# Optimization experiments

Hardware: AMD Instinct MI355X
Metric: run time of the kernel (lower is better)

The kernel has to match this reference:

```python
import jax, jax.numpy as jnp
import numpy as np
from jax import lax

THETA = 1.0      # neuron['theta']
TAU_SR = 10.0    # neuron['tauSr'] (SRM synaptic time constant)
TAU_RHO = 1.0    # surrogate-gradient width
SCALE_RHO = 1.0  # surrogate-gradient scale
T_SIM = 100      # simulation['tSample']


def srm_kernel(T, dtype=jnp.float32):
    t = jnp.arange(T, dtype=dtype)
    return (t / TAU_SR) * jnp.exp(1.0 - t / TAU_SR)  # eps(0)=0, peak 1 at t=tau


def psp(x, eps):
    """Causal temporal filter along last axis: y[t] = sum_k eps[k] * x[t-k]."""
    shape = x.shape
    T = shape[-1]
    xf = x.reshape(-1, 1, T)
    k = eps[::-1].reshape(1, 1, T)
    y = lax.conv_general_dilated(xf, k, (1,), [(T - 1, 0)],
                                 dimension_numbers=('NCH', 'OIH', 'NCH'))
    return y.reshape(shape)


def spike(u):
    return (u >= THETA).astype(u.dtype)


def conv_t(x, w, pad):
    """Per-timestep 2D conv. x:[B,C,H,W,T], w:[O,I,kh,kw] -> [B,O,H',W',T]."""
    B, C, H, W, T = x.shape
    xt = jnp.moveaxis(x, -1, 1).reshape(B * T, C, H, W)
    y = lax.conv_general_dilated(xt, w, (1, 1), [(pad, pad), (pad, pad)],
                                 dimension_numbers=('NCHW', 'OIHW', 'NCHW'))
    O, Ho, Wo = y.shape[1], y.shape[2], y.shape[3]
    return jnp.moveaxis(y.reshape(B, T, O, Ho, Wo), 1, -1)


def pool2(x):
    """SLAYER pool: 2x2 sum with fixed weight 1.1. x:[B,C,H,W,T]."""
    B, C, H, W, T = x.shape
    xr = x.reshape(B, C, H // 2, 2, W // 2, 2, T)
    return 1.1 * xr.sum(axis=(3, 5))


def dense_t(x, w):
    """x:[B,C,H,W,T] flattened over CHW; w:[O, C*H*W] -> [B,O,T]."""
    B = x.shape[0]
    T = x.shape[-1]
    xf = x.reshape(B, -1, T)
    return jnp.einsum('bit,oi->bot', xf, w)


def setup_inputs() -> dict:
    key = jax.random.key(0)
    k = jax.random.split(key, 6)
    img = jax.random.uniform(k[0], (32, 1, 28, 28), dtype=jnp.float32)
    rand_u = jax.random.uniform(k[1], (32, 1, 28, 28, T_SIM), dtype=jnp.float32)
    w1 = jax.random.normal(k[2], (16, 1, 5, 5), dtype=jnp.float32) * 0.2
    w2 = jax.random.normal(k[3], (32, 16, 5, 5), dtype=jnp.float32) * 0.05
    wf1 = jax.random.normal(k[4], (410, 1568), dtype=jnp.float32) * 0.05
    wf2 = jax.random.normal(k[5], (10, 410), dtype=jnp.float32) * 0.05
    return {"img": img, "rand_u": rand_u, "w1": w1, "w2": w2, "wf1": wf1, "wf2": wf2}


def reference(img, rand_u, w1, w2, wf1, wf2):
    eps = srm_kernel(T_SIM, img.dtype)
    # rate encoding: Bernoulli spikes with p = pixel intensity
    x = (rand_u < img[..., None]).astype(img.dtype)          # [B,1,28,28,T]
    x = spike(psp(conv_t(x, w1, 2), eps))                    # [B,16,28,28,T]
    x = spike(psp(pool2(x), eps))                            # [B,16,14,14,T]
    x = spike(psp(conv_t(x, w2, 2), eps))                    # [B,32,14,14,T]
    x = spike(psp(pool2(x), eps))                            # [B,32,7,7,T]
    x = spike(psp(dense_t(x, wf1), eps))                     # [B,410,T]
    x = spike(psp(jnp.einsum('bit,oi->bot', x, wf2), eps))   # [B,10,T]
    return x
```

## Files before the change

kernel.cpp:

```cpp
#include <hip/hip_runtime.h>


namespace {
constexpr int B = 32, T = 100;
constexpr double A1 = 0.90483741803595957;
constexpr double CE = 0.27182818284590452;
constexpr double SC39 = 549755813888.0;
constexpr double INV39 = 1.0 / 549755813888.0;

constexpr size_t OFF_M1 = 0;
constexpr size_t OFF_M2 = OFF_M1 + (size_t)B * T * 28 * 4;
constexpr size_t OFF_S4 = OFF_M2 + (size_t)B * T * 224 * 4;
constexpr size_t OFF_D5 = OFF_S4 + (size_t)B * T * 1568;
constexpr size_t OFF_S5 = OFF_D5 + (size_t)B * T * 410 * 8;
constexpr size_t OFF_D6 = OFF_S5 + (size_t)B * T * 410;
constexpr size_t OFF_BP = OFF_D6 + (size_t)B * T * 10 * 8;
constexpr size_t OFF_AP = OFF_D5;
}

using i32x4 = __attribute__((ext_vector_type(4))) int;
using i32x16 = __attribute__((ext_vector_type(16))) int;

__global__ void k_encode_pack(const float* __restrict__ img, const float* __restrict__ ru,
                              unsigned int* __restrict__ m1) {
  int i = blockIdx.x * 256 + threadIdx.x;
  if (i >= B * 28 * T) return;
  int t = i % T;
  int y = (i / T) % 28;
  int b = i / (T * 28);
  unsigned int m = 0;
  const float* rb = ru + ((size_t)b * 784 + y * 28) * T + t;
  const float* ib = img + b * 784 + y * 28;
  for (int x = 0; x < 28; x++) {
    m |= (rb[(size_t)x * T] < ib[x]) ? (1u << x) : 0u;
  }
  m1[((size_t)b * T + t) * 28 + y] = m;
}

__global__ __launch_bounds__(256) void k_conv1w(const unsigned int* __restrict__ m1,
                                                const float* __restrict__ w1,
                                                unsigned int* __restrict__ m2) {
  __shared__ double lut2[320 * 2];
  __shared__ unsigned int mrow[2][32];
  int o = blockIdx.x % 16, b = blockIdx.x / 16;
  int tid = threadIdx.x;
  for (int e = tid; e < 320; e += 256) {
    int dy = e / 64, f = e % 64;
    const float* wb = w1 + o * 25 + dy * 5;
    double v0 = 0.0, v1 = 0.0;
#pragma unroll
    for (int dx = 0; dx < 5; dx++) {
      double wv = (double)wb[dx];
      if ((f >> dx) & 1) v0 += wv;
      if ((f >> (dx + 1)) & 1) v1 += wv;
    }
    lut2[e * 2 + 0] = v0;
    lut2[e * 2 + 1] = v1;
  }
  if (tid < 32) {
    mrow[0][tid] = 0;
    mrow[1][tid] = 0;
  }
  int py = tid >> 4, px = tid & 15;
  bool act = (px < 14) && (py < 14);
  int yA = 2 * py, xA = 2 * px;
  double g1[4] = {0, 0, 0, 0}, g2[4] = {0, 0, 0, 0};
  double q1 = 0.0, q2 = 0.0;
  const unsigned int* m1b = m1 + (size_t)b * T * 28;
  if (tid < 28) mrow[0][tid + 2] = m1b[tid] << 2;
  __syncthreads();
  for (int t = 0; t < T; t++) {
    int p = t & 1, np = p ^ 1;
    bool dold = (tid < 28) && (t + 1 < T);
    unsigned int ldv = 0;
    if (dold) ldv = m1b[(t + 1) * 28 + tid] << 2;
    unsigned int poolBit = 0;
    if (act) {
      double sAa = 0, sAb = 0, sBa = 0, sBb = 0;
      const unsigned int* mc = mrow[p];
#pragma unroll
      for (int dy = 0; dy < 5; dy++) {
        unsigned int mA = mc[yA + dy];
        unsigned int mB = mc[yA + 1 + dy];
        const double* eA = lut2 + (dy * 64 + (int)((mA >> xA) & 63u)) * 2;
        const double* eB = lut2 + (dy * 64 + (int)((mB >> xA) & 63u)) * 2;
        sAa += eA[0];
        sAb += eA[1];
        sBa += eB[0];
        sBb += eB[1];
      }
      g1[0] = sAa + A1 * g1[0]; g2[0] = g1[0] + A1 * g2[0];
      g1[1] = sAb + A1 * g1[1]; g2[1] = g1[1] + A1 * g2[1];
      g1[2] = sBa + A1 * g1[2]; g2[2] = g1[2] + A1 * g2[2];
      g1[3] = sBb + A1 * g1[3]; g2[3] = g1[3] + A1 * g2[3];
      int s0 = (CE * (g2[0] - g1[0]) >= 1.0) ? 1 : 0;
      int s1 = (CE * (g2[1] - g1[1]) >= 1.0) ? 1 : 0;
      int s2 = (CE * (g2[2] - g1[2]) >= 1.0) ? 1 : 0;
      int s3 = (CE * (g2[3] - g1[3]) >= 1.0) ? 1 : 0;
      double s = 1.1 * (double)(s0 + s1 + s2 + s3);
      q1 = s + A1 * q1;
      q2 = q1 + A1 * q2;
      poolBit = (CE * (q2 - q1) >= 1.0) ? 1u : 0u;
    }
    unsigned long long bal = __ballot((int)poolBit);
    if (act && px == 0) {
      int lane = tid & 63;
      unsigned int rm = (unsigned int)((bal >> (lane & 48)) & 0x3FFFull);
      m2[((size_t)(b * T + t) * 16 + o) * 14 + py] = rm;
    }
    if (dold) mrow[np][tid + 2] = ldv;
    __syncthreads();
  }
}

__global__ void k_limbs(const float* __restrict__ w2, signed char* __restrict__ AP) {
  int i = blockIdx.x * 256 + threadIdx.x;
  if (i >= 32 * 80 * 8) return;
  int dx = i & 7;
  int g = (i >> 3) % 80;
  int o = i / 640;
  int c = g >> 2, r = g & 3, eh = r >> 1, kh = r & 1;
  int lane = kh * 32 + o, e = eh * 8 + dx;
  int ci = g / 5, dy = g % 5;
  float wv = (dx < 5) ? w2[((o * 16 + ci) * 5 + dy) * 5 + dx] : 0.0f;
  long long m = llrint((double)wv * SC39);
#pragma unroll
  for (int j = 0; j < 5; j++) {
    int d = (int)((m + 128) & 255) - 128;
    AP[(size_t)((j * 20 + c) * 64 + lane) * 16 + e] = (signed char)d;
    m = (m - d) >> 8;
  }
}

__global__ __launch_bounds__(512, 2) void k_conv2w(const unsigned int* __restrict__ m2,
                                                   const signed char* __restrict__ AP,
                                                   unsigned char* __restrict__ s4) {
  __shared__ unsigned int maskW[2][2][192];
  __shared__ double part[2][4][32][30];
  int yp = blockIdx.x % 7, b = blockIdx.x / 7;
  int y0 = yp * 2;
  int tid = threadIdx.x;
  int w = tid >> 6, l = tid & 63;
  int tp = w & 1, kq = w >> 1;
  int col = l & 31, kh = l >> 5;
  int x = col % 14;
  unsigned int wmask = (col < 28) ? 31u : 0u;
  int half = (col >= 14) ? 1 : 0;
  const unsigned int* m2b = m2 + (size_t)b * T * 224;

  const i32x4* APv = (const i32x4*)AP;
  i32x4 Af[5][5];
#pragma unroll
  for (int j = 0; j < 5; j++)
#pragma unroll
    for (int q = 0; q < 5; q++)
      Af[j][q] = APv[(size_t)(j * 20 + 5 * kq + q) * 64 + l];

  int stPos[3] = {-1, -1, -1}, stIdx[3] = {-1, -1, -1};
  if (w < 2) {
#pragma unroll
    for (int pass = 0; pass < 3; pass++) {
      if (pass == 2 && l >= 32) continue;
      int e = pass * 64 + l;
      int H = e / 80, g = e % 80;
      int c = g >> 2, eh2 = (g >> 1) & 1, kh2 = g & 1;
      int kq2 = c / 5, q2 = c % 5;
      int ci = g / 5, dy = g % 5;
      int iy = y0 - 2 + H + dy;
      stPos[pass] = H * 96 + kh2 * 48 + kq2 * 12 + q2 * 2 + eh2;
      if (iy >= 0 && iy < 14) stIdx[pass] = ci * 14 + iy;
    }
  }

  int ct = tid - 256;
  bool chainAct = (ct >= 0) && (ct < 224);
  int po = (ct >= 0) ? ct / 7 : 0;
  int pp = (ct >= 0) ? ct % 7 : 0;
  double sg1[4] = {0, 0, 0, 0}, sg2[4] = {0, 0, 0, 0};
  double pq1 = 0.0, pq2 = 0.0;

  if (w < 2) {
#pragma unroll
    for (int pass = 0; pass < 3; pass++) {
      if (stPos[pass] < 0) continue;
      unsigned int v = 0;
      if (stIdx[pass] >= 0) v = m2b[(size_t)w * 224 + stIdx[pass]] << 2;
      maskW[0][w][stPos[pass]] = v;
    }
  }
  __syncthreads();

  for (int grp = 0; grp < 50; grp++) {
    int p = grp & 1, np = p ^ 1;

    unsigned int ld0 = 0, ld1 = 0, ld2 = 0;
    bool doStage = (w < 2) && (grp + 1 < 50);
    if (doStage) {
      size_t tb = (size_t)((grp + 1) * 2 + w) * 224;
      if (stIdx[0] >= 0) ld0 = m2b[tb + stIdx[0]] << 2;
      if (stIdx[1] >= 0) ld1 = m2b[tb + stIdx[1]] << 2;
      if (stIdx[2] >= 0) ld2 = m2b[tb + stIdx[2]] << 2;
    }

    {
      const uint4* mwv = (const uint4*)&maskW[p][tp][0];
      int base4 = half * 24 + kh * 12 + kq * 3;
      uint4 mk0 = mwv[base4 + 0], mk1 = mwv[base4 + 1], mk2 = mwv[base4 + 2];
      i32x16 ac0, ac1, ac2, ac3, ac4;
#pragma unroll
      for (int r = 0; r < 16; r++) { ac0[r] = 0; ac1[r] = 0; ac2[r] = 0; ac3[r] = 0; ac4[r] = 0; }
#pragma unroll
      for (int q = 0; q < 5; q++) {
        unsigned int ra = (q == 0) ? mk0.x : (q == 1) ? mk0.z : (q == 2) ? mk1.x
                         : (q == 3) ? mk1.z : mk2.x;
        unsigned int rb = (q == 0) ? mk0.y : (q == 1) ? mk0.w : (q == 2) ? mk1.y
                         : (q == 3) ? mk1.w : mk2.y;
        unsigned int a5 = (ra >> x) & wmask;
        unsigned int b5 = (rb >> x) & wmask;
        i32x4 bb;
        bb[0] = (int)(((a5 & 15u) * 0x204081u) & 0x01010101u);
        bb[1] = (int)((a5 >> 4) & 1u);
        bb[2] = (int)(((b5 & 15u) * 0x204081u) & 0x01010101u);
        bb[3] = (int)((b5 >> 4) & 1u);
        ac0 = __builtin_amdgcn_mfma_i32_32x32x32_i8(Af[0][q], bb, ac0, 0, 0, 0);
        ac1 = __builtin_amdgcn_mfma_i32_32x32x32_i8(Af[1][q], bb, ac1, 0, 0, 0);
        ac2 = __builtin_amdgcn_mfma_i32_32x32x32_i8(Af[2][q], bb, ac2, 0, 0, 0);
        ac3 = __builtin_amdgcn_mfma_i32_32x32x32_i8(Af[3][q], bb, ac3, 0, 0, 0);
        ac4 = __builtin_amdgcn_mfma_i32_32x32x32_i8(Af[4][q], bb, ac4, 0, 0, 0);
      }
      if (col < 28) {
#pragma unroll
        for (int r = 0; r < 16; r++) {
          int R = (r & 3) + 8 * (r >> 2) + 4 * kh;
          int c01 = ac1[r] * 256 + ac0[r];
          int c23 = ac3[r] * 256 + ac2[r];
          double S = ((double)ac4[r] * 65536.0 + (double)c23) * 65536.0 + (double)c01;
          part[tp][kq][R][col] = S;
        }
      }
    }

    if (doStage) {
      if (stPos[0] >= 0) maskW[np][w][stPos[0]] = ld0;
      if (stPos[1] >= 0) maskW[np][w][stPos[1]] = ld1;
      if (stPos[2] >= 0) maskW[np][w][stPos[2]] = ld2;
    }
    __syncthreads();

    if (chainAct) {
#pragma unroll
      for (int g = 0; g < 2; g++) {
        const double* q0a = &part[g][0][po][2 * pp];
        const double* q1a = &part[g][1][po][2 * pp];
        const double* q2a = &part[g][2][po][2 * pp];
        const double* q3a = &part[g][3][po][2 * pp];
        const double* q0b = &part[g][0][po][14 + 2 * pp];
        const double* q1b = &part[g][1][po][14 + 2 * pp];
        const double* q2b = &part[g][2][po][14 + 2 * pp];
        const double* q3b = &part[g][3][po][14 + 2 * pp];
        double c0 = ((q0a[0] + q1a[0]) + (q2a[0] + q3a[0])) * INV39;
        double c1 = ((q0a[1] + q1a[1]) + (q2a[1] + q3a[1])) * INV39;
        double c2 = ((q0b[0] + q1b[0]) + (q2b[0] + q3b[0])) * INV39;
        double c3 = ((q0b[1] + q1b[1]) + (q2b[1] + q3b[1])) * INV39;
        sg1[0] = c0 + A1 * sg1[0]; sg2[0] = sg1[0] + A1 * sg2[0];
        sg1[1] = c1 + A1 * sg1[1]; sg2[1] = sg1[1] + A1 * sg2[1];
        sg1[2] = c2 + A1 * sg1[2]; sg2[2] = sg1[2] + A1 * sg2[2];
        sg1[3] = c3 + A1 * sg1[3]; sg2[3] = sg1[3] + A1 * sg2[3];
        int sum = ((CE * (sg2[0] - sg1[0]) >= 1.0) ? 1 : 0)
                + ((CE * (sg2[1] - sg1[1]) >= 1.0) ? 1 : 0)
                + ((CE * (sg2[2] - sg1[2]) >= 1.0) ? 1 : 0)
                + ((CE * (sg2[3] - sg1[3]) >= 1.0) ? 1 : 0);
        double s = 1.1 * (double)sum;
        pq1 = s + A1 * pq1;
        pq2 = pq1 + A1 * pq2;
        s4[(size_t)(b * T + grp * 2 + g) * 1568 + po * 49 + yp * 7 + pp] =
            (CE * (pq2 - pq1) >= 1.0) ? 1 : 0;
      }
    }
    __syncthreads();
  }
}

__global__ void k_limbs2(const float* __restrict__ wf1, signed char* __restrict__ BP) {
  int i = blockIdx.x * 256 + threadIdx.x;
  if (i >= 13 * 5 * 49 * 64) return;
  int lane = i & 63;
  int fi = i >> 6;
  int c = fi % 49;
  int j = (fi / 49) % 5;
  int ot = fi / 245;
  int o = ot * 32 + (lane & 31);
  int kb = 32 * c + (lane >> 5) * 16;
  int wd[4] = {0, 0, 0, 0};
#pragma unroll
  for (int e = 0; e < 16; e++) {
    float wv = (o < 410) ? wf1[(size_t)o * 1568 + kb + e] : 0.0f;
    long long m = llrint((double)wv * SC39);
    int d = 0;
    for (int jj = 0; jj <= j; jj++) {
      d = (int)((m + 128) & 255) - 128;
      m = (m - d) >> 8;
    }
    wd[e >> 2] |= (d & 255) << ((e & 3) * 8);
  }
  i32x4 v;
  v[0] = wd[0]; v[1] = wd[1]; v[2] = wd[2]; v[3] = wd[3];
  *(i32x4*)(BP + (size_t)i * 16) = v;
}

__global__ __launch_bounds__(256) void k_dense1m(const unsigned char* __restrict__ s4,
                                                 const signed char* __restrict__ BP,
                                                 double* __restrict__ d5) {
  int ot = blockIdx.y;
  int w = threadIdx.x >> 6, l = threadIdx.x & 63;
  int col = l & 31, kh = l >> 5;
  int btTile = blockIdx.x * 4 + w;
  const unsigned char* arow = s4 + (size_t)(btTile * 32 + col) * 1568 + kh * 16;
  const i32x4* bpv = (const i32x4*)BP + (size_t)ot * 245 * 64 + l;
  i32x16 acc0, acc1, acc2, acc3, acc4;
#pragma unroll
  for (int r = 0; r < 16; r++) {
    acc0[r] = 0; acc1[r] = 0; acc2[r] = 0; acc3[r] = 0; acc4[r] = 0;
  }
  for (int c = 0; c < 49; c++) {
    i32x4 a = *(const i32x4*)(arow + 32 * c);
    i32x4 b0 = bpv[(0 * 49 + c) * 64];
    i32x4 b1 = bpv[(1 * 49 + c) * 64];
    i32x4 b2 = bpv[(2 * 49 + c) * 64];
    i32x4 b3 = bpv[(3 * 49 + c) * 64];
    i32x4 b4 = bpv[(4 * 49 + c) * 64];
    acc0 = __builtin_amdgcn_mfma_i32_32x32x32_i8(a, b0, acc0, 0, 0, 0);
    acc1 = __builtin_amdgcn_mfma_i32_32x32x32_i8(a, b1, acc1, 0, 0, 0);
    acc2 = __builtin_amdgcn_mfma_i32_32x32x32_i8(a, b2, acc2, 0, 0, 0);
    acc3 = __builtin_amdgcn_mfma_i32_32x32x32_i8(a, b3, acc3, 0, 0, 0);
    acc4 = __builtin_amdgcn_mfma_i32_32x32x32_i8(a, b4, acc4, 0, 0, 0);
  }
  int o = ot * 32 + col;
  if (o < 410) {
#pragma unroll
    for (int r = 0; r < 16; r++) {
      int R = (r & 3) + 8 * (r >> 2) + 4 * kh;
      double v = ((((double)acc4[r] * 256.0 + (double)acc3[r]) * 256.0 +
                   (double)acc2[r]) * 256.0 + (double)acc1[r]) * 256.0 + (double)acc0[r];
      d5[(size_t)(btTile * 32 + R) * 410 + o] = v * INV39;
    }
  }
}

__global__ void k_psp5(const double* __restrict__ d5, unsigned char* __restrict__ s5) {
  int tid = blockIdx.x * 256 + threadIdx.x;
  if (tid >= B * 410) return;
  int o = tid % 410, b = tid / 410;
  double g1 = 0.0, g2 = 0.0;
  for (int t = 0; t < T; t++) {
    double s = d5[(size_t)(b * T + t) * 410 + o];
    g1 = s + A1 * g1;
    g2 = g1 + A1 * g2;
    s5[(size_t)(b * T + t) * 410 + o] = (CE * (g2 - g1) >= 1.0) ? 1 : 0;
  }
}

__global__ void k_dense2(const unsigned char* __restrict__ s5, const float* __restrict__ wf2,
                         double* __restrict__ d6) {
  int tid = blockIdx.x * 256 + threadIdx.x;
  if (tid >= B * T * 10) return;
  int o = tid % 10, bt = tid / 10;
  const unsigned char* sr = s5 + (size_t)bt * 410;
  const float* wr = wf2 + o * 410;
  double s = 0.0;
  for (int i = 0; i < 410; i++) s += (double)wr[i] * (double)sr[i];
  d6[tid] = s;
}

__global__ void k_psp6(const double* __restrict__ d6, float* __restrict__ out) {
  int tid = blockIdx.x * 256 + threadIdx.x;
  if (tid >= B * 10) return;
  int o = tid % 10, b = tid / 10;
  double g1 = 0.0, g2 = 0.0;
  for (int t = 0; t < T; t++) {
    double s = d6[(size_t)(b * T + t) * 10 + o];
    g1 = s + A1 * g1;
    g2 = g1 + A1 * g2;
    out[(size_t)b * 1000 + o * 100 + t] = (CE * (g2 - g1) >= 1.0) ? 1.0f : 0.0f;
  }
}

extern "C" void kernel_launch(void* const* d_in, const int* in_sizes, int n_in,
                              void* d_out, int out_size, void* d_ws, size_t ws_size,
                              hipStream_t stream) {
  const float* img = (const float*)d_in[0];
  const float* ru = (const float*)d_in[1];
  const float* w1 = (const float*)d_in[2];
  const float* w2 = (const float*)d_in[3];
  const float* wf1 = (const float*)d_in[4];
  const float* wf2 = (const float*)d_in[5];

  unsigned char* ws = (unsigned char*)d_ws;
  unsigned int* m1 = (unsigned int*)(ws + OFF_M1);
  unsigned int* m2 = (unsigned int*)(ws + OFF_M2);
  unsigned char* s4 = ws + OFF_S4;
  double* d5 = (double*)(ws + OFF_D5);
  unsigned char* s5 = ws + OFF_S5;
  double* d6 = (double*)(ws + OFF_D6);
  signed char* AP = (signed char*)(ws + OFF_AP);
  signed char* BP = (signed char*)(ws + OFF_BP);
  float* out = (float*)d_out;

  k_encode_pack<<<(B * 28 * T + 255) / 256, 256, 0, stream>>>(img, ru, m1);
  k_limbs<<<(32 * 80 * 8 + 255) / 256, 256, 0, stream>>>(w2, AP);
  k_limbs2<<<(13 * 5 * 49 * 64 + 255) / 256, 256, 0, stream>>>(wf1, BP);
  k_conv1w<<<B * 16, 256, 0, stream>>>(m1, w1, m2);
  k_conv2w<<<B * 7, 512, 0, stream>>>(m2, AP, s4);
  k_dense1m<<<dim3(25, 13), 256, 0, stream>>>(s4, BP, d5);
  k_psp5<<<(B * 410 + 255) / 256, 256, 0, stream>>>(d5, s5);
  k_dense2<<<(B * T * 10 + 255) / 256, 256, 0, stream>>>(s5, wf2, d6);
  k_psp6<<<2, 256, 0, stream>>>(d6, out);
}
```

Baseline: 353.5 us.

## Reduce conv2 K-quarter partials with LDS int64 atomics and double-buffer partials

The conv2 kernel's four K-quarter waves now atomically add exact 64-bit integer partial sums into a shared, double-buffered accumulator. Previously each wave wrote separate double partials that the chain threads then summed. Double-buffering by group parity lets the second barrier per iteration be dropped, and the chain threads clear their slots after reading them. The aim is to cut LDS footprint and barrier stalls, in exchange for LDS atomic contention and 64-bit atomic cost.

```diff
diff --git a/kernel.cpp b/kernel.cpp
--- a/kernel.cpp
+++ b/kernel.cpp
@@ -132,11 +132,11 @@
   }
 }
 
-__global__ __launch_bounds__(512, 2) void k_conv2w(const unsigned int* __restrict__ m2,
+__global__ __launch_bounds__(512, 2) void k_conv2v(const unsigned int* __restrict__ m2,
                                                    const signed char* __restrict__ AP,
                                                    unsigned char* __restrict__ s4) {
   __shared__ unsigned int maskW[2][2][192];
-  __shared__ double part[2][4][32][30];
+  __shared__ unsigned long long part[2][2][32][30];
   int yp = blockIdx.x % 7, b = blockIdx.x / 7;
   int y0 = yp * 2;
   int tid = threadIdx.x;
@@ -179,6 +179,10 @@
   double sg1[4] = {0, 0, 0, 0}, sg2[4] = {0, 0, 0, 0};
   double pq1 = 0.0, pq2 = 0.0;
 
+  {
+    unsigned long long* pf = &part[0][0][0][0];
+    for (int e = tid; e < 2 * 2 * 32 * 30; e += 512) pf[e] = 0ull;
+  }
   if (w < 2) {
 #pragma unroll
     for (int pass = 0; pass < 3; pass++) {
@@ -234,8 +238,9 @@
           int R = (r & 3) + 8 * (r >> 2) + 4 * kh;
           int c01 = ac1[r] * 256 + ac0[r];
           int c23 = ac3[r] * 256 + ac2[r];
-          double S = ((double)ac4[r] * 65536.0 + (double)c23) * 65536.0 + (double)c01;
-          part[tp][kq][R][col] = S;
+          long long S = (long long)ac4[r] * 4294967296LL +
+                        (long long)c23 * 65536LL + (long long)c01;
+          atomicAdd(&part[p][tp][R][col], (unsigned long long)S);
         }
       }
     }
@@ -250,18 +255,18 @@
     if (chainAct) {
 #pragma unroll
       for (int g = 0; g < 2; g++) {
-        const double* q0a = &part[g][0][po][2 * pp];
-        const double* q1a = &part[g][1][po][2 * pp];
-        const double* q2a = &part[g][2][po][2 * pp];
-        const double* q3a = &part[g][3][po][2 * pp];
-        const double* q0b = &part[g][0][po][14 + 2 * pp];
-        const double* q1b = &part[g][1][po][14 + 2 * pp];
-        const double* q2b = &part[g][2][po][14 + 2 * pp];
-        const double* q3b = &part[g][3][po][14 + 2 * pp];
-        double c0 = ((q0a[0] + q1a[0]) + (q2a[0] + q3a[0])) * INV39;
-        double c1 = ((q0a[1] + q1a[1]) + (q2a[1] + q3a[1])) * INV39;
-        double c2 = ((q0b[0] + q1b[0]) + (q2b[0] + q3b[0])) * INV39;
-        double c3 = ((q0b[1] + q1b[1]) + (q2b[1] + q3b[1])) * INV39;
+        unsigned long long v0 = part[p][g][po][2 * pp];
+        unsigned long long v1 = part[p][g][po][2 * pp + 1];
+        unsigned long long v2 = part[p][g][po][14 + 2 * pp];
+        unsigned long long v3 = part[p][g][po][15 + 2 * pp];
+        part[p][g][po][2 * pp] = 0ull;
+        part[p][g][po][2 * pp + 1] = 0ull;
+        part[p][g][po][14 + 2 * pp] = 0ull;
+        part[p][g][po][15 + 2 * pp] = 0ull;
+        double c0 = (double)(long long)v0 * INV39;
+        double c1 = (double)(long long)v1 * INV39;
+        double c2 = (double)(long long)v2 * INV39;
+        double c3 = (double)(long long)v3 * INV39;
         sg1[0] = c0 + A1 * sg1[0]; sg2[0] = sg1[0] + A1 * sg2[0];
         sg1[1] = c1 + A1 * sg1[1]; sg2[1] = sg1[1] + A1 * sg2[1];
         sg1[2] = c2 + A1 * sg1[2]; sg2[2] = sg1[2] + A1 * sg2[2];
@@ -277,7 +282,6 @@
             (CE * (pq2 - pq1) >= 1.0) ? 1 : 0;
       }
     }
-    __syncthreads();
   }
 }
 
@@ -410,7 +414,7 @@
   k_limbs<<<(32 * 80 * 8 + 255) / 256, 256, 0, stream>>>(w2, AP);
   k_limbs2<<<(13 * 5 * 49 * 64 + 255) / 256, 256, 0, stream>>>(wf1, BP);
   k_conv1w<<<B * 16, 256, 0, stream>>>(m1, w1, m2);
-  k_conv2w<<<B * 7, 512, 0, stream>>>(m2, AP, s4);
+  k_conv2v<<<B * 7, 512, 0, stream>>>(m2, AP, s4);
   k_dense1m<<<dim3(25, 13), 256, 0, stream>>>(s4, BP, d5);
   k_psp5<<<(B * 410 + 255) / 256, 256, 0, stream>>>(d5, s5);
   k_dense2<<<(B * T * 10 + 255) / 256, 256, 0, stream>>>(s5, wf2, d6);
```

Result: faster. 345.5 us (-2.3%).
